# Performance work log

Measured on AMD Instinct MI355X. Metric: run time of the kernel, lower is better.

The kernel has to match this reference:

```python
import jax, jax.numpy as jnp
import numpy as np

N_NODES = 10000
N_EDGES = 320000
D_NODE = 128
D_EDGE = 32
D_IN = 2 * D_NODE + D_EDGE  # 288, concat(sender, receiver, edge)
D_HID = 192                 # AutoMLP log-spaced hidden dim between 288 and 128
D_OUT = 128


def setup_inputs() -> dict:
    key = jax.random.key(0)
    ks = jax.random.split(key, 8)
    n_embed = jax.random.normal(ks[0], (N_NODES, D_NODE), dtype=jnp.float32)
    e_embed = jax.random.normal(ks[1], (N_EDGES, D_EDGE), dtype=jnp.float32)
    senders = jnp.sort(jax.random.randint(ks[2], (N_EDGES,), 0, N_NODES, dtype=jnp.int32))
    receivers = jax.random.randint(ks[3], (N_EDGES,), 0, N_NODES, dtype=jnp.int32)
    # AutoMLP parameters (lecun_normal-style scaling)
    W1 = jax.random.normal(ks[4], (D_IN, D_HID), dtype=jnp.float32) / np.sqrt(D_IN)
    b1 = jnp.zeros((D_HID,), dtype=jnp.float32)
    W2 = jax.random.normal(ks[5], (D_HID, D_OUT), dtype=jnp.float32) / np.sqrt(D_HID)
    b2 = jnp.zeros((D_OUT,), dtype=jnp.float32)
    return {"n_embed": n_embed, "e_embed": e_embed, "senders": senders,
            "receivers": receivers, "W1": W1, "b1": b1, "W2": W2, "b2": b2}


def reference(n_embed, e_embed, senders, receivers, W1, b1, W2, b2):
    # gather sender/receiver node embeddings and concat with edge features: [E, 288]
    inp = jnp.concatenate([n_embed[senders], n_embed[receivers], e_embed], axis=-1)
    # AutoMLP: Dense -> tanh -> Dense (final layer linear)
    h = jnp.tanh(inp @ W1 + b1)          # [E, 192]
    msg = h @ W2 + b2                    # [E, 128]
    # segment_mean over senders (sorted), num_segments = n_nodes
    seg_sum = jax.ops.segment_sum(msg, senders, num_segments=N_NODES,
                                  indices_are_sorted=True)
    counts = jax.ops.segment_sum(jnp.ones((msg.shape[0],), dtype=msg.dtype), senders,
                                 num_segments=N_NODES, indices_are_sorted=True)
    return seg_sum / jnp.maximum(counts, 1.0)[:, None]
```

## Files before the change

kernel.cpp:

```cpp
#include <hip/hip_runtime.h>

#define E_TOT 320000
#define NN    10000
#define DN    128
#define DE    32
#define DH    192
#define DO    128
#define EB    64
#define SHS   196

typedef __attribute__((ext_vector_type(8))) short bf16x8;
typedef __attribute__((ext_vector_type(4))) float f32x4;

#define E_FRAGS  (12*64)
#define W2_FRAGS (6*8*64)
#define FRAGS_TOT (E_FRAGS + W2_FRAGS)
#define ZH (NN * DH / 4)
#define PREP_ITEMS (FRAGS_TOT + ZH + E_TOT)
#define NPROJ (((NN + 63) / 64) * 2)
__device__ __align__(16) unsigned short g_e [E_FRAGS * 8];
__device__ __align__(16) unsigned short g_p2[W2_FRAGS * 8];

__device__ __forceinline__ unsigned short f2bf(float f) {
    union { float f; unsigned u; } v; v.f = f;
    return (unsigned short)((v.u + 0x7FFFu + ((v.u >> 16) & 1u)) >> 16);
}
__device__ __forceinline__ float bflo(unsigned u) {
    union { unsigned v; float f; } t; t.v = u << 16; return t.f;
}
__device__ __forceinline__ float bfhi(unsigned u) {
    union { unsigned v; float f; } t; t.v = u & 0xFFFF0000u; return t.f;
}
__device__ __forceinline__ float bf2f(unsigned short s) {
    union { unsigned v; float f; } t; t.v = (unsigned)s << 16; return t.f;
}
__device__ __forceinline__ float tanh_fast(float x) {
    float ex = __expf(x + x);
    return 1.0f - 2.0f * __builtin_amdgcn_rcpf(ex + 1.0f);
}
__device__ __forceinline__ unsigned cvt_pk_bf16(float lo, float hi) {
    unsigned r;
    asm("v_cvt_pk_bf16_f32 %0, %1, %2" : "=v"(r) : "v"(lo), "v"(hi));
    return r;
}

__global__ __launch_bounds__(256) void prep_proj(
    const float* __restrict__ n_embed, const float* __restrict__ W1,
    const float* __restrict__ W2, const float* __restrict__ b1,
    const int* __restrict__ senders,
    unsigned short* __restrict__ P, float* __restrict__ Hbar,
    int* __restrict__ row_start)
{
    __shared__ __align__(16) unsigned short s_a[64][136];
    const int tid = threadIdx.x;

    if (blockIdx.x >= NPROJ) {
        int f = (blockIdx.x - NPROJ) * 256 + tid;
        unsigned short tmp[8];
        if (f < E_FRAGS) {
            int mt = f >> 6, lane = f & 63;
            int k0 = ((lane >> 4) << 3);
            int hid = mt * 16 + (lane & 15);
            #pragma unroll
            for (int i = 0; i < 8; ++i) tmp[i] = f2bf(W1[(256 + k0 + i) * DH + hid]);
            *(uint4*)(g_e + (size_t)f * 8) = *(const uint4*)tmp;
        } else if (f < FRAGS_TOT) {
            int f3 = f - E_FRAGS;
            int kk = f3 / (8 * 64), nt = (f3 >> 6) % 8, lane = f3 & 63;
            int r0 = kk * 32 + ((lane >> 4) << 3);
            int c  = nt * 16 + (lane & 15);
            #pragma unroll
            for (int i = 0; i < 8; ++i) tmp[i] = f2bf(W2[(r0 + i) * DO + c]);
            *(uint4*)(g_p2 + (size_t)f3 * 8) = *(const uint4*)tmp;
        } else if (f < FRAGS_TOT + ZH) {
            ((float4*)Hbar)[f - FRAGS_TOT] = make_float4(0.f, 0.f, 0.f, 0.f);
        } else if (f < PREP_ITEMS) {
            int e = f - FRAGS_TOT - ZH;
            int s_cur  = senders[e];
            int s_prev = (e == 0) ? -1 : senders[e - 1];
            if (s_prev != s_cur)
                for (int n = s_prev + 1; n <= s_cur; ++n) row_start[n] = e;
            if (e == E_TOT - 1)
                for (int n = s_cur + 1; n <= NN; ++n) row_start[n] = E_TOT;
        }
        return;
    }

    const int half = blockIdx.x & 1;
    const int n0   = (blockIdx.x >> 1) * 64;

    #pragma unroll
    for (int it = 0; it < 8; ++it) {
        int idx = tid + it * 256;
        int row = idx >> 5, c = idx & 31;
        float4 v = make_float4(0.f, 0.f, 0.f, 0.f);
        if (n0 + row < NN) v = ((const float4*)(n_embed + (size_t)(n0 + row) * DN))[c];
        unsigned t0 = cvt_pk_bf16(v.x, v.y), t1 = cvt_pk_bf16(v.z, v.w);
        *(uint2*)&s_a[row][c * 4] = make_uint2(t0, t1);
    }
    __syncthreads();

    const int lane = tid & 63, w = tid >> 6;
    const int arow = lane & 15, akb = (lane >> 4) * 8, rbase = (lane >> 4) * 4;

    f32x4 acc[4][3];
    #pragma unroll
    for (int mt = 0; mt < 4; ++mt)
        #pragma unroll
        for (int j = 0; j < 3; ++j) acc[mt][j] = (f32x4){0.f, 0.f, 0.f, 0.f};

    for (int kk = 0; kk < 4; ++kk) {
        bf16x8 a[4];
        union { bf16x8 v; unsigned short t[8]; } b[3];
        #pragma unroll
        for (int mt = 0; mt < 4; ++mt)
            a[mt] = *(const bf16x8*)&s_a[mt * 16 + arow][kk * 32 + akb];
        #pragma unroll
        for (int j = 0; j < 3; ++j) {
            const int r0 = (kk + 4 * half) * 32 + akb;
            const int c  = (3 * w + j) * 16 + arow;
            #pragma unroll
            for (int i = 0; i < 8; ++i) b[j].t[i] = f2bf(W1[(size_t)(r0 + i) * DH + c]);
        }
        #pragma unroll
        for (int mt = 0; mt < 4; ++mt)
            #pragma unroll
            for (int j = 0; j < 3; ++j)
                acc[mt][j] = __builtin_amdgcn_mfma_f32_16x16x32_bf16(a[mt], b[j].v, acc[mt][j], 0, 0, 0);
    }

    unsigned short* Pout = P + (size_t)half * NN * DH;
    float bj[3];
    #pragma unroll
    for (int j = 0; j < 3; ++j) bj[j] = (half == 0) ? b1[48 * w + 16 * j + arow] : 0.f;
    const int gq = arow >> 2, ii = arow & 3;
    #pragma unroll
    for (int mt = 0; mt < 4; ++mt)
        #pragma unroll
        for (int j = 0; j < 3; ++j)
            #pragma unroll
            for (int r = 0; r < 4; ++r) {
                int row = n0 + mt * 16 + rbase + r;
                if (row < NN)
                    Pout[((size_t)row * 4 + gq) * 48 + (3 * w + j) * 4 + ii] =
                        f2bf(acc[mt][j][r] + bj[j]);
            }
}

__global__ __launch_bounds__(256) void edge_reduce(
    const float* __restrict__ e_embed,
    const int* __restrict__ senders, const int* __restrict__ receivers,
    const unsigned short* __restrict__ Ps, const unsigned short* __restrict__ Pr,
    float* __restrict__ Hbar)
{
    __shared__ __align__(16) unsigned short s_h[EB][SHS];
    __shared__ int s_send[EB];

    const int tid  = threadIdx.x;
    const int nb8  = gridDim.x >> 3;
    const int e0   = (((blockIdx.x & 7) * nb8) + (blockIdx.x >> 3)) * EB;
    const int lane = tid & 63, w = tid >> 6;
    const int arow = lane & 15, g = lane >> 4;

    const int myedge = e0 + w * 16 + arow;
    const int sN = senders[myedge], rN = receivers[myedge];
    const unsigned short* psbase = Ps + ((size_t)sN * 4 + g) * 48;
    const unsigned short* prbase = Pr + ((size_t)rN * 4 + g) * 48;
    uint4 psq[6], prq[6];
    #pragma unroll
    for (int j = 0; j < 6; ++j) {
        psq[j] = *(const uint4*)(psbase + j * 8);
        prq[j] = *(const uint4*)(prbase + j * 8);
    }
    union { bf16x8 v; unsigned u[4]; } bfr;
    {
        const float* erow = e_embed + (size_t)myedge * DE + g * 8;
        float4 ev0 = *(const float4*)erow;
        float4 ev1 = *(const float4*)(erow + 4);
        bfr.u[0] = cvt_pk_bf16(ev0.x, ev0.y);
        bfr.u[1] = cvt_pk_bf16(ev0.z, ev0.w);
        bfr.u[2] = cvt_pk_bf16(ev1.x, ev1.y);
        bfr.u[3] = cvt_pk_bf16(ev1.z, ev1.w);
    }
    if (tid < EB) s_send[tid] = senders[e0 + tid];

    #pragma unroll
    for (int mt = 0; mt < 12; ++mt) {
        unsigned px, py, qx, qy;
        if ((mt & 1) == 0) {
            px = psq[mt >> 1].x; py = psq[mt >> 1].y;
            qx = prq[mt >> 1].x; qy = prq[mt >> 1].y;
        } else {
            px = psq[mt >> 1].z; py = psq[mt >> 1].w;
            qx = prq[mt >> 1].z; qy = prq[mt >> 1].w;
        }
        f32x4 cinit;
        cinit[0] = bflo(px) + bflo(qx);
        cinit[1] = bfhi(px) + bfhi(qx);
        cinit[2] = bflo(py) + bflo(qy);
        cinit[3] = bfhi(py) + bfhi(qy);
        bf16x8 af = *(const bf16x8*)(g_e + ((size_t)mt * 64 + lane) * 8);
        f32x4 acc = __builtin_amdgcn_mfma_f32_16x16x32_bf16(af, bfr.v, cinit, 0, 0, 0);
        float t0 = tanh_fast(acc[0]);
        float t1 = tanh_fast(acc[1]);
        float t2 = tanh_fast(acc[2]);
        float t3 = tanh_fast(acc[3]);
        *(uint2*)&s_h[w * 16 + arow][mt * 16 + g * 4] =
            make_uint2(cvt_pk_bf16(t0, t1), cvt_pk_bf16(t2, t3));
    }
    __syncthreads();

    if (tid < DH) {
        const int c = tid;
        float sum = 0.f;
        int cur = s_send[0];
        #pragma unroll 8
        for (int e = 0; e < EB; ++e) {
            sum += bf2f(s_h[e][c]);
            int nxt = (e + 1 < EB) ? s_send[e + 1] : -1;
            if (nxt != cur) {
                atomicAdd(&Hbar[(size_t)cur * DH + c], sum);
                sum = 0.f;
                cur = nxt;
            }
        }
    }
}

__global__ __launch_bounds__(256) void node_out(
    const float* __restrict__ Hbar, const int* __restrict__ row_start,
    const float* __restrict__ b2, float* __restrict__ out)
{
    const int tid  = threadIdx.x;
    const int lane = tid & 63, w = tid >> 6;
    const int n0   = (blockIdx.x * 4 + w) * 16;
    if (n0 >= NN) return;
    const int arow = lane & 15, akb = (lane >> 4) * 8, rbase = (lane >> 4) * 4;

    const int myrow = (n0 + arow < NN) ? (n0 + arow) : (NN - 1);
    const int cnt = row_start[myrow + 1] - row_start[myrow];
    const float ic = (cnt > 0) ? 1.0f / (float)cnt : 0.0f;

    const float* hrow = Hbar + (size_t)myrow * DH;
    union { bf16x8 v; unsigned u[4]; } a[6];
    #pragma unroll
    for (int kk = 0; kk < 6; ++kk) {
        float4 v0 = *(const float4*)(hrow + kk * 32 + akb);
        float4 v1 = *(const float4*)(hrow + kk * 32 + akb + 4);
        a[kk].u[0] = cvt_pk_bf16(v0.x * ic, v0.y * ic);
        a[kk].u[1] = cvt_pk_bf16(v0.z * ic, v0.w * ic);
        a[kk].u[2] = cvt_pk_bf16(v1.x * ic, v1.y * ic);
        a[kk].u[3] = cvt_pk_bf16(v1.z * ic, v1.w * ic);
    }

    f32x4 acc[8];
    #pragma unroll
    for (int j = 0; j < 8; ++j) acc[j] = (f32x4){0.f, 0.f, 0.f, 0.f};

    #pragma unroll
    for (int kk = 0; kk < 6; ++kk)
        #pragma unroll
        for (int j = 0; j < 8; ++j) {
            bf16x8 b = *(const bf16x8*)(g_p2 + (((size_t)kk * 8 + j) * 64 + lane) * 8);
            acc[j] = __builtin_amdgcn_mfma_f32_16x16x32_bf16(a[kk].v, b, acc[j], 0, 0, 0);
        }

    #pragma unroll
    for (int j = 0; j < 8; ++j) {
        const float bd = b2[j * 16 + arow];
        #pragma unroll
        for (int r = 0; r < 4; ++r) {
            int row = n0 + rbase + r;
            if (row < NN)
                out[(size_t)row * DO + j * 16 + arow] = acc[j][r] + bd;
        }
    }
}

extern "C" void kernel_launch(void* const* d_in, const int* in_sizes, int n_in,
                              void* d_out, int out_size, void* d_ws, size_t ws_size,
                              hipStream_t stream)
{
    const float* n_embed   = (const float*)d_in[0];
    const float* e_embed   = (const float*)d_in[1];
    const int*   senders   = (const int*)d_in[2];
    const int*   receivers = (const int*)d_in[3];
    const float* W1        = (const float*)d_in[4];
    const float* b1        = (const float*)d_in[5];
    const float* W2        = (const float*)d_in[6];
    const float* b2        = (const float*)d_in[7];
    float* out = (float*)d_out;

    unsigned short* Ps   = (unsigned short*)d_ws;
    unsigned short* Pr   = Ps + (size_t)NN * DH;
    float*          Hbar = (float*)(Pr + (size_t)NN * DH);
    int*            row_start = (int*)(Hbar + (size_t)NN * DH);

    const int prep_blocks = (PREP_ITEMS + 255) / 256;
    prep_proj<<<NPROJ + prep_blocks, 256, 0, stream>>>(
        n_embed, W1, W2, b1, senders, Ps, Hbar, row_start);
    edge_reduce<<<E_TOT / EB, 256, 0, stream>>>(
        e_embed, senders, receivers, Ps, Pr, Hbar);
    node_out<<<(NN + 63) / 64, 256, 0, stream>>>(Hbar, row_start, b2, out);
}
```

Measured before the change: 75.47 us.

## Process two edge tiles per block, prefetching second gather during first reduce

Each edge_reduce block now handles two 64-edge tiles. The second tile's sender/receiver projection gather is issued before the first tile's segment reduction, so gather latency overlaps the atomic reduction. The grid is halved and the XCD-aware block remapping is generalised to grid sizes not divisible by 8. In exchange, holding two gather buffers in registers raises register pressure and may lower occupancy, and the extra barriers serialise the phases inside each block.

```diff
diff --git a/kernel.cpp b/kernel.cpp
--- a/kernel.cpp
+++ b/kernel.cpp
@@ -147,52 +147,49 @@
             }
 }
 
-__global__ __launch_bounds__(256) void edge_reduce(
+struct Gather {
+    uint4 psq[6], prq[6];
+    union { bf16x8 v; unsigned u[4]; } bfr;
+};
+
+__device__ __forceinline__ void issue_gather(
+    int e0, int lane, int w, int arow, int g,
     const float* __restrict__ e_embed,
     const int* __restrict__ senders, const int* __restrict__ receivers,
     const unsigned short* __restrict__ Ps, const unsigned short* __restrict__ Pr,
-    float* __restrict__ Hbar)
-{
-    __shared__ __align__(16) unsigned short s_h[EB][SHS];
-    __shared__ int s_send[EB];
-
-    const int tid  = threadIdx.x;
-    const int nb8  = gridDim.x >> 3;
-    const int e0   = (((blockIdx.x & 7) * nb8) + (blockIdx.x >> 3)) * EB;
-    const int lane = tid & 63, w = tid >> 6;
-    const int arow = lane & 15, g = lane >> 4;
-
+    Gather& gt)
+{
     const int myedge = e0 + w * 16 + arow;
     const int sN = senders[myedge], rN = receivers[myedge];
     const unsigned short* psbase = Ps + ((size_t)sN * 4 + g) * 48;
     const unsigned short* prbase = Pr + ((size_t)rN * 4 + g) * 48;
-    uint4 psq[6], prq[6];
     #pragma unroll
     for (int j = 0; j < 6; ++j) {
-        psq[j] = *(const uint4*)(psbase + j * 8);
-        prq[j] = *(const uint4*)(prbase + j * 8);
-    }
-    union { bf16x8 v; unsigned u[4]; } bfr;
-    {
-        const float* erow = e_embed + (size_t)myedge * DE + g * 8;
-        float4 ev0 = *(const float4*)erow;
-        float4 ev1 = *(const float4*)(erow + 4);
-        bfr.u[0] = cvt_pk_bf16(ev0.x, ev0.y);
-        bfr.u[1] = cvt_pk_bf16(ev0.z, ev0.w);
-        bfr.u[2] = cvt_pk_bf16(ev1.x, ev1.y);
-        bfr.u[3] = cvt_pk_bf16(ev1.z, ev1.w);
-    }
-    if (tid < EB) s_send[tid] = senders[e0 + tid];
-
+        gt.psq[j] = *(const uint4*)(psbase + j * 8);
+        gt.prq[j] = *(const uint4*)(prbase + j * 8);
+    }
+    const float* erow = e_embed + (size_t)myedge * DE + g * 8;
+    float4 ev0 = *(const float4*)erow;
+    float4 ev1 = *(const float4*)(erow + 4);
+    gt.bfr.u[0] = cvt_pk_bf16(ev0.x, ev0.y);
+    gt.bfr.u[1] = cvt_pk_bf16(ev0.z, ev0.w);
+    gt.bfr.u[2] = cvt_pk_bf16(ev1.x, ev1.y);
+    gt.bfr.u[3] = cvt_pk_bf16(ev1.z, ev1.w);
+}
+
+__device__ __forceinline__ void phase1_tile(
+    const Gather& gt, int lane, int w, int arow, int g,
+    unsigned short (*s_h)[SHS])
+{
     #pragma unroll
     for (int mt = 0; mt < 12; ++mt) {
         unsigned px, py, qx, qy;
         if ((mt & 1) == 0) {
-            px = psq[mt >> 1].x; py = psq[mt >> 1].y;
-            qx = prq[mt >> 1].x; qy = prq[mt >> 1].y;
+            px = gt.psq[mt >> 1].x; py = gt.psq[mt >> 1].y;
+            qx = gt.prq[mt >> 1].x; qy = gt.prq[mt >> 1].y;
         } else {
-            px = psq[mt >> 1].z; py = psq[mt >> 1].w;
-            qx = prq[mt >> 1].z; qy = prq[mt >> 1].w;
+            px = gt.psq[mt >> 1].z; py = gt.psq[mt >> 1].w;
+            qx = gt.prq[mt >> 1].z; qy = gt.prq[mt >> 1].w;
         }
         f32x4 cinit;
         cinit[0] = bflo(px) + bflo(qx);
@@ -200,7 +197,7 @@
         cinit[2] = bflo(py) + bflo(qy);
         cinit[3] = bfhi(py) + bfhi(qy);
         bf16x8 af = *(const bf16x8*)(g_e + ((size_t)mt * 64 + lane) * 8);
-        f32x4 acc = __builtin_amdgcn_mfma_f32_16x16x32_bf16(af, bfr.v, cinit, 0, 0, 0);
+        f32x4 acc = __builtin_amdgcn_mfma_f32_16x16x32_bf16(af, gt.bfr.v, cinit, 0, 0, 0);
         float t0 = tanh_fast(acc[0]);
         float t1 = tanh_fast(acc[1]);
         float t2 = tanh_fast(acc[2]);
@@ -208,8 +205,12 @@
         *(uint2*)&s_h[w * 16 + arow][mt * 16 + g * 4] =
             make_uint2(cvt_pk_bf16(t0, t1), cvt_pk_bf16(t2, t3));
     }
-    __syncthreads();
-
+}
+
+__device__ __forceinline__ void reduce_tile(
+    int tid, const int* s_send, unsigned short (*s_h)[SHS],
+    float* __restrict__ Hbar)
+{
     if (tid < DH) {
         const int c = tid;
         float sum = 0.f;
@@ -227,6 +228,46 @@
     }
 }
 
+__global__ __launch_bounds__(256) void edge_reduce(
+    const float* __restrict__ e_embed,
+    const int* __restrict__ senders, const int* __restrict__ receivers,
+    const unsigned short* __restrict__ Ps, const unsigned short* __restrict__ Pr,
+    float* __restrict__ Hbar)
+{
+    __shared__ __align__(16) unsigned short s_h[EB][SHS];
+    __shared__ int s_send[2][EB];
+
+    const int tid = threadIdx.x;
+    const int nwg = gridDim.x, q = nwg >> 3, r = nwg & 7;
+    const int xcd = blockIdx.x & 7, loc = blockIdx.x >> 3;
+    const int wg  = (xcd < r) ? (xcd * (q + 1) + loc)
+                              : (r * (q + 1) + (xcd - r) * q + loc);
+    const int e0  = wg * 2 * EB;
+    const int lane = tid & 63, w = tid >> 6;
+    const int arow = lane & 15, g = lane >> 4;
+
+    Gather ga;
+    issue_gather(e0, lane, w, arow, g, e_embed, senders, receivers, Ps, Pr, ga);
+    if (tid < EB) {
+        s_send[0][tid] = senders[e0 + tid];
+        s_send[1][tid] = senders[e0 + EB + tid];
+    }
+
+    phase1_tile(ga, lane, w, arow, g, s_h);
+    __syncthreads();
+
+    Gather gb;
+    issue_gather(e0 + EB, lane, w, arow, g, e_embed, senders, receivers, Ps, Pr, gb);
+
+    reduce_tile(tid, s_send[0], s_h, Hbar);
+    __syncthreads();
+
+    phase1_tile(gb, lane, w, arow, g, s_h);
+    __syncthreads();
+
+    reduce_tile(tid, s_send[1], s_h, Hbar);
+}
+
 __global__ __launch_bounds__(256) void node_out(
     const float* __restrict__ Hbar, const int* __restrict__ row_start,
     const float* __restrict__ b2, float* __restrict__ out)
@@ -299,7 +340,7 @@
     const int prep_blocks = (PREP_ITEMS + 255) / 256;
     prep_proj<<<NPROJ + prep_blocks, 256, 0, stream>>>(
         n_embed, W1, W2, b1, senders, Ps, Hbar, row_start);
-    edge_reduce<<<E_TOT / EB, 256, 0, stream>>>(
+    edge_reduce<<<E_TOT / (2 * EB), 256, 0, stream>>>(
         e_embed, senders, receivers, Ps, Pr, Hbar);
     node_out<<<(NN + 63) / 64, 256, 0, stream>>>(Hbar, row_start, b2, out);
 }
```

New measurement: 84.54 us. +12.0%, slower.
